# Kernel optimization log

Measured on AMD Instinct MI355X. Metric: run time of the kernel, lower is better.

Reference implementation:

```python
import jax, jax.numpy as jnp
import numpy as np

DIM = 1024
N_HEADS = 16


def setup_inputs() -> dict:
    key = jax.random.key(0)
    ks = jax.random.split(key, 7)
    x = jax.random.normal(ks[0], (2, 2048, DIM), dtype=jnp.float32)
    wq = jax.random.normal(ks[1], (DIM, DIM), dtype=jnp.float32) * 0.01
    wk = jax.random.normal(ks[2], (DIM, DIM), dtype=jnp.float32) * 0.01
    wv = jax.random.normal(ks[3], (DIM, DIM), dtype=jnp.float32) * 0.01
    wo = jax.random.normal(ks[4], (DIM, DIM), dtype=jnp.float32) * 0.01
    w1 = jax.random.normal(ks[5], (DIM, 4 * DIM), dtype=jnp.float32) * 0.01
    w2 = jax.random.normal(ks[6], (4 * DIM, DIM), dtype=jnp.float32) * 0.01
    return {"x": x, "wq": wq, "wk": wk, "wv": wv, "wo": wo, "w1": w1, "w2": w2}


def reference(x, wq, wk, wv, wo, w1, w2):
    bsz, seqlen, dim = x.shape
    head_dim = dim // N_HEADS
    # project and split heads: [b, h, s, d]
    q = (x @ wq).reshape(bsz, seqlen, N_HEADS, head_dim).transpose(0, 2, 1, 3)
    k = (x @ wk).reshape(bsz, seqlen, N_HEADS, head_dim).transpose(0, 2, 1, 3)
    v = (x @ wv).reshape(bsz, seqlen, N_HEADS, head_dim).transpose(0, 2, 1, 3)
    scale = head_dim ** (-0.5)
    # full [b, h, s, s] score matrix, as in the original module
    attn = jnp.einsum('bhqd,bhkd->bhqk', q, k) * scale
    attn = jax.nn.softmax(attn, axis=-1)
    out = jnp.einsum('bhqk,bhkd->bhqd', attn, v)
    out = out.transpose(0, 2, 1, 3).reshape(bsz, seqlen, dim)
    x = x + out @ wo
    h = jax.nn.relu(x @ w1)
    x = x + h @ w2
    return x
```

## Files before the change

kernel.cpp:

```cpp
#include <hip/hip_runtime.h>
#include <hip/hip_bf16.h>
#include <stdint.h>

typedef __attribute__((ext_vector_type(8))) short short8_t;
typedef __attribute__((ext_vector_type(4))) short short4_t;
typedef __attribute__((ext_vector_type(4))) float floatx4;

#define MTOT 4096
#define DIMV 1024
#define SEQ  2048
#define NH   16
#define HD   64
#define QKV_LD 3072
#define KVB 64
#define NKT (SEQ / KVB)

__device__ __forceinline__ floatx4 mfma16(short8_t a, short8_t b, floatx4 c) {
    return __builtin_amdgcn_mfma_f32_16x16x32_bf16(a, b, c, 0, 0, 0);
}

__device__ __forceinline__ void gload_lds16(const void* g, void* l) {
    __builtin_amdgcn_global_load_lds(
        (const __attribute__((address_space(1))) void*)g,
        (__attribute__((address_space(3))) void*)l,
        16, 0, 0);
}

__device__ __forceinline__ short bf16bits(float f) {
    return __builtin_bit_cast(short, __float2bfloat16(f));
}

__device__ __forceinline__ short8_t frag64(const __hip_bfloat16* base, int row, int col0) {
    int off = row * 64 + (((col0 >> 3) ^ (row & 7)) << 3);
    return *(const short8_t*)(base + off);
}

struct bf4 { __hip_bfloat16 a, b, c, d; };

__global__ void prep_all(const float* __restrict__ x,
                         const float* __restrict__ wq, const float* __restrict__ wk,
                         const float* __restrict__ wv, const float* __restrict__ wo,
                         const float* __restrict__ w1, const float* __restrict__ w2,
                         __hip_bfloat16* __restrict__ xb,
                         __hip_bfloat16* __restrict__ wqkvt, __hip_bfloat16* __restrict__ wot,
                         __hip_bfloat16* __restrict__ w1t, __hip_bfloat16* __restrict__ w2t) {
    __shared__ float tile[32][33];
    int bid = blockIdx.x;
    int t = threadIdx.x;
    if (bid >= 12288) {
        int i = (bid - 12288) * 256 + t;
        const float4* xv = reinterpret_cast<const float4*>(x) + i;
        float4 v = *xv;
        bf4 r;
        r.a = __float2bfloat16(v.x); r.b = __float2bfloat16(v.y);
        r.c = __float2bfloat16(v.z); r.d = __float2bfloat16(v.w);
        *reinterpret_cast<bf4*>(xb + (size_t)i * 4) = r;
        return;
    }
    const float* w; __hip_bfloat16* wt; int K, N, K32, tau; float scale = 1.0f;
    if (bid < 1024)      { w = wq; wt = wqkvt;                 K = 1024; N = 1024; K32 = 32;  tau = bid;        scale = 0.125f; }
    else if (bid < 2048) { w = wk; wt = wqkvt + 1024 * 1024;   K = 1024; N = 1024; K32 = 32;  tau = bid - 1024; }
    else if (bid < 3072) { w = wv; wt = wqkvt + 2048 * 1024;   K = 1024; N = 1024; K32 = 32;  tau = bid - 2048; }
    else if (bid < 4096) { w = wo; wt = wot;                   K = 1024; N = 1024; K32 = 32;  tau = bid - 3072; }
    else if (bid < 8192) { w = w1; wt = w1t;                   K = 1024; N = 4096; K32 = 32;  tau = bid - 4096; }
    else                 { w = w2; wt = w2t;                   K = 4096; N = 1024; K32 = 128; tau = bid - 8192; }
    int k0 = (tau % K32) * 32, n0 = (tau / K32) * 32;
    int tx = t & 31, ty = t >> 5;
    #pragma unroll
    for (int r = 0; r < 32; r += 8)
        tile[ty + r][tx] = w[(size_t)(k0 + ty + r) * N + n0 + tx];
    __syncthreads();
    #pragma unroll
    for (int r = 0; r < 32; r += 8)
        wt[(size_t)(n0 + ty + r) * K + k0 + tx] = __float2bfloat16(tile[tx][ty + r] * scale);
}

__global__ void vtrans(const __hip_bfloat16* __restrict__ v, int ld,
                       __hip_bfloat16* __restrict__ vt) {
    __shared__ __hip_bfloat16 tile[32][33];
    int s0 = blockIdx.x * 32;
    int c0 = blockIdx.y * 32;
    int tx = threadIdx.x & 31, ty = threadIdx.x >> 5;
    #pragma unroll
    for (int r = 0; r < 32; r += 8)
        tile[ty + r][tx] = v[(size_t)(s0 + ty + r) * ld + c0 + tx];
    __syncthreads();
    int b = s0 >> 11;
    int h = c0 >> 6;
    int d0 = c0 & 63;
    #pragma unroll
    for (int r = 0; r < 32; r += 8)
        vt[(size_t)((b * NH + h) * HD + d0 + ty + r) * SEQ + (s0 & 2047) + tx] = tile[tx][ty + r];
}

__global__ void combine2(const float* __restrict__ p0, const float* __restrict__ p1,
                         const float* __restrict__ resid, float* __restrict__ out, int n4) {
    int i = blockIdx.x * 256 + threadIdx.x;
    if (i < n4) {
        float4 a = reinterpret_cast<const float4*>(p0)[i];
        float4 b = reinterpret_cast<const float4*>(p1)[i];
        float4 c = reinterpret_cast<const float4*>(resid)[i];
        float4 r;
        r.x = a.x + b.x + c.x; r.y = a.y + b.y + c.y;
        r.z = a.z + b.z + c.z; r.w = a.w + b.w + c.w;
        reinterpret_cast<float4*>(out)[i] = r;
    }
}

template <int EPI>
__launch_bounds__(256)
__global__ void gemm_bt(const __hip_bfloat16* __restrict__ A,
                        const __hip_bfloat16* __restrict__ Bt,
                        int M, int N, int K, int lda, int ldb, float scale,
                        const float* __restrict__ resid,
                        float* __restrict__ outf,
                        __hip_bfloat16* __restrict__ outb, size_t zout) {
    __shared__ __align__(16) __hip_bfloat16 As[3][128 * 32];
    __shared__ __align__(16) __hip_bfloat16 Bs[3][128 * 32];
    A += (size_t)blockIdx.z * K;
    Bt += (size_t)blockIdx.z * K;
    outf += (size_t)blockIdx.z * zout;
    const int t = threadIdx.x;
    const int l = t & 63;
    const int w = t >> 6;
    const int wr = w >> 1, wc = w & 1;
    const int lrow = l & 15;
    const int lk = (l >> 4) << 3;
    const int li4 = (l >> 4) << 2;
    const int arow0 = blockIdx.x * 128;
    const int brow0 = blockIdx.y * 128;

    floatx4 acc[4][4];
    #pragma unroll
    for (int m = 0; m < 4; m++)
        #pragma unroll
        for (int n = 0; n < 4; n++)
            acc[m][n] = (floatx4){0.f, 0.f, 0.f, 0.f};

    const int nkt = K >> 5;
    const int sr = t >> 2, sc8 = (t & 3) << 3;
    const __hip_bfloat16* ga0 = A + (size_t)(arow0 + sr) * lda + sc8;
    const __hip_bfloat16* gb0 = Bt + (size_t)(brow0 + sr) * ldb + sc8;

#define GSTAGE(KT, BUF) do { \
        const __hip_bfloat16* ga_ = ga0 + (KT) * 32; \
        const __hip_bfloat16* gb_ = gb0 + (KT) * 32; \
        gload_lds16(ga_,                    (char*)As[BUF] + t * 16); \
        gload_lds16(ga_ + (size_t)64 * lda, (char*)As[BUF] + 4096 + t * 16); \
        gload_lds16(gb_,                    (char*)Bs[BUF] + t * 16); \
        gload_lds16(gb_ + (size_t)64 * ldb, (char*)Bs[BUF] + 4096 + t * 16); \
    } while (0)

    GSTAGE(0, 0);
    GSTAGE(1, 1);
    asm volatile("s_waitcnt vmcnt(4)" ::: "memory");
    __builtin_amdgcn_s_barrier();
    __builtin_amdgcn_sched_barrier(0);

    for (int kt = 0; kt < nkt; ++kt) {
        const int cur = kt % 3;
        if (kt + 2 < nkt) GSTAGE(kt + 2, (kt + 2) % 3);
        short8_t af[4], bfr[4];
        #pragma unroll
        for (int m = 0; m < 4; m++)
            af[m] = *(const short8_t*)((const char*)As[cur] + (((wr << 6) + (m << 4) + lrow) << 6) + (lk << 1));
        #pragma unroll
        for (int n = 0; n < 4; n++)
            bfr[n] = *(const short8_t*)((const char*)Bs[cur] + (((wc << 6) + (n << 4) + lrow) << 6) + (lk << 1));
        #pragma unroll
        for (int m = 0; m < 4; m++)
            #pragma unroll
            for (int n = 0; n < 4; n++)
                acc[m][n] = mfma16(af[m], bfr[n], acc[m][n]);
        if (kt + 2 < nkt) asm volatile("s_waitcnt vmcnt(4)" ::: "memory");
        else              asm volatile("s_waitcnt vmcnt(0)" ::: "memory");
        __builtin_amdgcn_s_barrier();
        __builtin_amdgcn_sched_barrier(0);
    }
#undef GSTAGE

    #pragma unroll
    for (int m = 0; m < 4; m++) {
        #pragma unroll
        for (int n = 0; n < 4; n++) {
            int row = arow0 + (wr << 6) + (m << 4) + li4;
            int col = brow0 + (wc << 6) + (n << 4) + lrow;
            #pragma unroll
            for (int i = 0; i < 4; i++) {
                float vv = acc[m][n][i] * scale;
                size_t off = (size_t)(row + i) * N + col;
                if (EPI == 0) {
                    outb[off] = __float2bfloat16(vv);
                } else if (EPI == 1) {
                    outb[off] = __float2bfloat16(vv > 0.f ? vv : 0.f);
                } else if (EPI == 2) {
                    float f = vv + resid[off];
                    outf[off] = f;
                    outb[off] = __float2bfloat16(f);
                } else if (EPI == 3) {
                    outf[off] = vv + resid[off];
                } else {
                    outf[off] = vv;
                }
            }
        }
    }
}

__launch_bounds__(256, 4)
__global__ void attn_kernel(const __hip_bfloat16* __restrict__ qkv,
                            const __hip_bfloat16* __restrict__ vt,
                            __hip_bfloat16* __restrict__ o) {
    __shared__ __align__(16) __hip_bfloat16 Ks[2][KVB * 64];
    __shared__ __align__(16) __hip_bfloat16 Vs[2][KVB * 64];
    __shared__ __align__(16) __hip_bfloat16 Ps[64 * 64];
    const int t = threadIdx.x, l = t & 63, w = t >> 6;
    const int bh = blockIdx.y;
    const int b = bh >> 4, h = bh & 15;
    const int q0 = blockIdx.x * 64;
    const int lq = l & 15;
    const int lg = l >> 4;

    const __hip_bfloat16* qbase = qkv + (size_t)(b * SEQ + q0) * QKV_LD + h * HD;
    const __hip_bfloat16* kbase = qkv + (size_t)(b * SEQ) * QKV_LD + 1024 + h * HD;
    const __hip_bfloat16* vbase = vt + (size_t)(bh * HD) * SEQ;

    #pragma unroll
    for (int s = 0; s < 2; ++s) {
        int u = t + 256 * s;
        int r = u >> 3, c = (u & 7) ^ (r & 7);
        gload_lds16(qbase + (size_t)r * QKV_LD + c * 8, (char*)Ps + u * 16);
        gload_lds16(kbase + (size_t)r * QKV_LD + c * 8, (char*)Ks[0] + u * 16);
        gload_lds16(vbase + (size_t)r * SEQ + c * 8,    (char*)Vs[0] + u * 16);
    }
    asm volatile("s_waitcnt vmcnt(0)" ::: "memory");
    __builtin_amdgcn_s_barrier();
    __builtin_amdgcn_sched_barrier(0);

    short8_t qf[2];
    #pragma unroll
    for (int kc = 0; kc < 2; kc++)
        qf[kc] = frag64(Ps, (w << 4) + lq, kc * 32 + lg * 8);
    asm volatile("s_waitcnt lgkmcnt(0)" ::: "memory");
    __builtin_amdgcn_s_barrier();
    __builtin_amdgcn_sched_barrier(0);

    float l_part = 0.f;
    floatx4 o_acc[4];
    #pragma unroll
    for (int n = 0; n < 4; n++)
        o_acc[n] = (floatx4){0.f, 0.f, 0.f, 0.f};

    int cur = 0;
    for (int kt = 0; kt < NKT; ++kt) {
        if (kt + 1 < NKT) {
            int kv = (kt + 1) * KVB;
            #pragma unroll
            for (int s = 0; s < 2; ++s) {
                int u = t + 256 * s;
                int r = u >> 3, c = (u & 7) ^ (r & 7);
                gload_lds16(kbase + (size_t)(kv + r) * QKV_LD + c * 8,
                            (char*)Ks[cur ^ 1] + u * 16);
                gload_lds16(vbase + (size_t)r * SEQ + kv + c * 8,
                            (char*)Vs[cur ^ 1] + u * 16);
            }
        }

        const __hip_bfloat16* kcb = Ks[cur];
        floatx4 sa[4];
        #pragma unroll
        for (int n = 0; n < 4; n++)
            sa[n] = (floatx4){0.f, 0.f, 0.f, 0.f};
        #pragma unroll
        for (int n = 0; n < 4; n++) {
            #pragma unroll
            for (int kc = 0; kc < 2; kc++) {
                short8_t kf = frag64(kcb, n * 16 + lq, kc * 32 + lg * 8);
                sa[n] = mfma16(kf, qf[kc], sa[n]);
            }
        }

        short4_t pk[4];
        #pragma unroll
        for (int n = 0; n < 4; n++) {
            float p0 = __expf(sa[n][0]);
            float p1 = __expf(sa[n][1]);
            float p2 = __expf(sa[n][2]);
            float p3 = __expf(sa[n][3]);
            l_part += (p0 + p1) + (p2 + p3);
            short4_t pv;
            pv[0] = bf16bits(p0);
            pv[1] = bf16bits(p1);
            pv[2] = bf16bits(p2);
            pv[3] = bf16bits(p3);
            pk[n] = pv;
        }

        {
            int row = (w << 4) + lq;
            int rowb = row * 128;
            int rw = row & 7;
            #pragma unroll
            for (int n = 0; n < 4; n++) {
                int k0 = n * 16 + lg * 4;
                char* dst = (char*)Ps + rowb +
                            ((((k0 >> 3) ^ rw) << 4) | ((k0 & 4) << 1));
                *(short4_t*)dst = pk[n];
            }
        }
        asm volatile("s_waitcnt lgkmcnt(0)" ::: "memory");
        __builtin_amdgcn_sched_barrier(0);

        const __hip_bfloat16* vcb = Vs[cur];
        #pragma unroll
        for (int kc = 0; kc < 2; kc++) {
            short8_t pf = frag64(Ps, (w << 4) + lq, kc * 32 + lg * 8);
            #pragma unroll
            for (int n = 0; n < 4; n++) {
                short8_t vf = frag64(vcb, n * 16 + lq, kc * 32 + lg * 8);
                o_acc[n] = mfma16(pf, vf, o_acc[n]);
            }
        }
        asm volatile("s_waitcnt vmcnt(0)" ::: "memory");
        __builtin_amdgcn_s_barrier();
        __builtin_amdgcn_sched_barrier(0);
        cur ^= 1;
    }

    __hip_bfloat16* obase = o + (size_t)(b * SEQ + q0) * DIMV + h * HD;
    float lr = l_part;
    lr += __shfl_xor(lr, 16, 64);
    lr += __shfl_xor(lr, 32, 64);
    #pragma unroll
    for (int i = 0; i < 4; i++) {
        float li = 1.0f / __shfl(lr, (lg << 2) + i, 16);
        int row = (w << 4) + (lg << 2) + i;
        #pragma unroll
        for (int n = 0; n < 4; n++) {
            obase[(size_t)row * DIMV + n * 16 + lq] =
                __float2bfloat16(o_acc[n][i] * li);
        }
    }
}

extern "C" void kernel_launch(void* const* d_in, const int* in_sizes, int n_in,
                              void* d_out, int out_size, void* d_ws, size_t ws_size,
                              hipStream_t stream) {
    const float* x  = (const float*)d_in[0];
    const float* wq = (const float*)d_in[1];
    const float* wk = (const float*)d_in[2];
    const float* wv = (const float*)d_in[3];
    const float* wo = (const float*)d_in[4];
    const float* w1 = (const float*)d_in[5];
    const float* w2 = (const float*)d_in[6];
    float* outf = (float*)d_out;

    char* ws = (char*)d_ws;
    const size_t MB = (size_t)1 << 20;
    __hip_bfloat16* xb    = (__hip_bfloat16*)(ws + 0 * MB);
    __hip_bfloat16* wqkvt = (__hip_bfloat16*)(ws + 8 * MB);
    __hip_bfloat16* wot   = (__hip_bfloat16*)(ws + 14 * MB);
    __hip_bfloat16* w1t   = (__hip_bfloat16*)(ws + 16 * MB);
    __hip_bfloat16* w2t   = (__hip_bfloat16*)(ws + 24 * MB);
    __hip_bfloat16* qkvb  = (__hip_bfloat16*)(ws + 32 * MB);
    __hip_bfloat16* vtp   = (__hip_bfloat16*)(ws + 56 * MB);
    __hip_bfloat16* atb   = (__hip_bfloat16*)(ws + 64 * MB);
    __hip_bfloat16* x1b   = (__hip_bfloat16*)(ws + 72 * MB);
    __hip_bfloat16* hb    = (__hip_bfloat16*)(ws + 80 * MB);
    float* part0 = (float*)(ws + 32 * MB);

    prep_all<<<dim3(16384), dim3(256), 0, stream>>>(x, wq, wk, wv, wo, w1, w2,
                                                    xb, wqkvt, wot, w1t, w2t);

    gemm_bt<0><<<dim3(32, 24), dim3(256), 0, stream>>>(xb, wqkvt, MTOT, QKV_LD, 1024,
                                                       1024, 1024, 1.0f, nullptr, nullptr, qkvb, 0);
    vtrans<<<dim3(128, 32), dim3(256), 0, stream>>>(qkvb + 2048, QKV_LD, vtp);

    attn_kernel<<<dim3(32, 32), dim3(256), 0, stream>>>(qkvb, vtp, atb);

    gemm_bt<2><<<dim3(32, 8), dim3(256), 0, stream>>>(atb, wot, MTOT, 1024, 1024,
                                                      1024, 1024, 1.0f, x, outf, x1b, 0);
    gemm_bt<1><<<dim3(32, 32), dim3(256), 0, stream>>>(x1b, w1t, MTOT, 4096, 1024,
                                                       1024, 1024, 1.0f, nullptr, nullptr, hb, 0);
    gemm_bt<4><<<dim3(32, 8, 2), dim3(256), 0, stream>>>(hb, w2t, MTOT, 1024, 2048,
                                                         4096, 4096, 1.0f, nullptr, part0, nullptr,
                                                         (size_t)MTOT * 1024);
    combine2<<<dim3(4096), dim3(256), 0, stream>>>(part0, part0 + (size_t)MTOT * 1024,
                                                   outf, outf, MTOT * 1024 / 4);
}
```

Measured before the change: 340.9 us.

## Add 256x256-tile GEMM for QKV and FFN1, fold log2e into Q scale

```diff
diff --git a/kernel.cpp b/kernel.cpp
--- a/kernel.cpp
+++ b/kernel.cpp
@@ -14,6 +14,7 @@
 #define QKV_LD 3072
 #define KVB 64
 #define NKT (SEQ / KVB)
+#define LOG2E 1.44269504088896340736f
 
 __device__ __forceinline__ floatx4 mfma16(short8_t a, short8_t b, floatx4 c) {
     return __builtin_amdgcn_mfma_f32_16x16x32_bf16(a, b, c, 0, 0, 0);
@@ -58,7 +59,7 @@
         return;
     }
     const float* w; __hip_bfloat16* wt; int K, N, K32, tau; float scale = 1.0f;
-    if (bid < 1024)      { w = wq; wt = wqkvt;                 K = 1024; N = 1024; K32 = 32;  tau = bid;        scale = 0.125f; }
+    if (bid < 1024)      { w = wq; wt = wqkvt;                 K = 1024; N = 1024; K32 = 32;  tau = bid;        scale = 0.125f * LOG2E; }
     else if (bid < 2048) { w = wk; wt = wqkvt + 1024 * 1024;   K = 1024; N = 1024; K32 = 32;  tau = bid - 1024; }
     else if (bid < 3072) { w = wv; wt = wqkvt + 2048 * 1024;   K = 1024; N = 1024; K32 = 32;  tau = bid - 2048; }
     else if (bid < 4096) { w = wo; wt = wot;                   K = 1024; N = 1024; K32 = 32;  tau = bid - 3072; }
@@ -104,6 +105,107 @@
         r.x = a.x + b.x + c.x; r.y = a.y + b.y + c.y;
         r.z = a.z + b.z + c.z; r.w = a.w + b.w + c.w;
         reinterpret_cast<float4*>(out)[i] = r;
+    }
+}
+
+template <int EPI>
+__launch_bounds__(512)
+__global__ void gemm256(const __hip_bfloat16* __restrict__ A,
+                        const __hip_bfloat16* __restrict__ Bt,
+                        int N, int K, int lda, int ldb,
+                        __hip_bfloat16* __restrict__ outb) {
+    __shared__ __align__(16) __hip_bfloat16 As[2][256 * 64];
+    __shared__ __align__(16) __hip_bfloat16 Bs[2][256 * 64];
+    const int t = threadIdx.x;
+    const int l = t & 63;
+    const int w = t >> 6;
+    const int wr = w >> 2;
+    const int wc = w & 3;
+    const int lq = l & 15;
+    const int lk = (l >> 4) << 3;
+    const int li4 = (l >> 4) << 2;
+    const int arow0 = blockIdx.x * 256;
+    const int brow0 = blockIdx.y * 256;
+
+    floatx4 acc[8][4];
+    #pragma unroll
+    for (int m = 0; m < 8; m++)
+        #pragma unroll
+        for (int n = 0; n < 4; n++)
+            acc[m][n] = (floatx4){0.f, 0.f, 0.f, 0.f};
+
+    const int sr_ = t >> 3;
+    const int sc_ = ((t & 7) ^ ((t >> 3) & 7));
+    const __hip_bfloat16* ga0 = A + (size_t)(arow0 + sr_) * lda + sc_ * 8;
+    const __hip_bfloat16* gb0 = Bt + (size_t)(brow0 + sr_) * ldb + sc_ * 8;
+
+#define STG_A(BUF, S, KT) gload_lds16(ga0 + (size_t)(64 * (S)) * lda + (KT) * 64, \
+                                      (char*)As[BUF] + (t + 512 * (S)) * 16)
+#define STG_B(BUF, S, KT) gload_lds16(gb0 + (size_t)(64 * (S)) * ldb + (KT) * 64, \
+                                      (char*)Bs[BUF] + (t + 512 * (S)) * 16)
+
+    const int nkt = K >> 6;
+    #pragma unroll
+    for (int s = 0; s < 4; ++s) { STG_A(0, s, 0); STG_B(0, s, 0); }
+    asm volatile("s_waitcnt vmcnt(0)" ::: "memory");
+    __builtin_amdgcn_s_barrier();
+    __builtin_amdgcn_sched_barrier(0);
+
+    for (int kt = 0; kt < nkt; ++kt) {
+        const int cur = kt & 1;
+        const bool pre = (kt + 1 < nkt);
+        #pragma unroll
+        for (int p = 0; p < 4; ++p) {
+            const int mh = p >> 1, nh = p & 1;
+            short8_t af[4][2], bf[2][2];
+            #pragma unroll
+            for (int mi = 0; mi < 4; mi++)
+                #pragma unroll
+                for (int kc = 0; kc < 2; kc++)
+                    af[mi][kc] = frag64(As[cur], wr * 128 + (mh * 4 + mi) * 16 + lq, kc * 32 + lk);
+            #pragma unroll
+            for (int ni = 0; ni < 2; ni++)
+                #pragma unroll
+                for (int kc = 0; kc < 2; kc++)
+                    bf[ni][kc] = frag64(Bs[cur], wc * 64 + (nh * 2 + ni) * 16 + lq, kc * 32 + lk);
+            if (pre) { STG_A(cur ^ 1, p, kt + 1); STG_B(cur ^ 1, p, kt + 1); }
+            __builtin_amdgcn_s_barrier();
+            asm volatile("s_waitcnt lgkmcnt(0)" ::: "memory");
+            __builtin_amdgcn_sched_barrier(0);
+            __builtin_amdgcn_s_setprio(1);
+            #pragma unroll
+            for (int kc = 0; kc < 2; kc++)
+                #pragma unroll
+                for (int mi = 0; mi < 4; mi++)
+                    #pragma unroll
+                    for (int ni = 0; ni < 2; ni++)
+                        acc[mh * 4 + mi][nh * 2 + ni] =
+                            mfma16(af[mi][kc], bf[ni][kc], acc[mh * 4 + mi][nh * 2 + ni]);
+            __builtin_amdgcn_s_setprio(0);
+            if (p == 3) {
+                if (pre) asm volatile("s_waitcnt vmcnt(0)" ::: "memory");
+            }
+            __builtin_amdgcn_s_barrier();
+            __builtin_amdgcn_sched_barrier(0);
+        }
+    }
+#undef STG_A
+#undef STG_B
+
+    #pragma unroll
+    for (int m = 0; m < 8; m++) {
+        #pragma unroll
+        for (int n = 0; n < 4; n++) {
+            int row = arow0 + wr * 128 + m * 16 + li4;
+            int col = brow0 + wc * 64 + n * 16 + lq;
+            #pragma unroll
+            for (int i = 0; i < 4; i++) {
+                float vv = acc[m][n][i];
+                size_t off = (size_t)(row + i) * N + col;
+                if (EPI == 0) outb[off] = __float2bfloat16(vv);
+                else          outb[off] = __float2bfloat16(vv > 0.f ? vv : 0.f);
+            }
+        }
     }
 }
 
@@ -191,14 +293,10 @@
                 size_t off = (size_t)(row + i) * N + col;
                 if (EPI == 0) {
                     outb[off] = __float2bfloat16(vv);
-                } else if (EPI == 1) {
-                    outb[off] = __float2bfloat16(vv > 0.f ? vv : 0.f);
                 } else if (EPI == 2) {
                     float f = vv + resid[off];
                     outf[off] = f;
                     outb[off] = __float2bfloat16(f);
-                } else if (EPI == 3) {
-                    outf[off] = vv + resid[off];
                 } else {
                     outf[off] = vv;
                 }
@@ -283,10 +381,10 @@
         short4_t pk[4];
         #pragma unroll
         for (int n = 0; n < 4; n++) {
-            float p0 = __expf(sa[n][0]);
-            float p1 = __expf(sa[n][1]);
-            float p2 = __expf(sa[n][2]);
-            float p3 = __expf(sa[n][3]);
+            float p0 = exp2f(sa[n][0]);
+            float p1 = exp2f(sa[n][1]);
+            float p2 = exp2f(sa[n][2]);
+            float p3 = exp2f(sa[n][3]);
             l_part += (p0 + p1) + (p2 + p3);
             short4_t pv;
             pv[0] = bf16bits(p0);
@@ -372,16 +470,14 @@
     prep_all<<<dim3(16384), dim3(256), 0, stream>>>(x, wq, wk, wv, wo, w1, w2,
                                                     xb, wqkvt, wot, w1t, w2t);
 
-    gemm_bt<0><<<dim3(32, 24), dim3(256), 0, stream>>>(xb, wqkvt, MTOT, QKV_LD, 1024,
-                                                       1024, 1024, 1.0f, nullptr, nullptr, qkvb, 0);
+    gemm256<0><<<dim3(16, 12), dim3(512), 0, stream>>>(xb, wqkvt, QKV_LD, 1024, 1024, 1024, qkvb);
     vtrans<<<dim3(128, 32), dim3(256), 0, stream>>>(qkvb + 2048, QKV_LD, vtp);
 
     attn_kernel<<<dim3(32, 32), dim3(256), 0, stream>>>(qkvb, vtp, atb);
 
     gemm_bt<2><<<dim3(32, 8), dim3(256), 0, stream>>>(atb, wot, MTOT, 1024, 1024,
                                                       1024, 1024, 1.0f, x, outf, x1b, 0);
-    gemm_bt<1><<<dim3(32, 32), dim3(256), 0, stream>>>(x1b, w1t, MTOT, 4096, 1024,
-                                                       1024, 1024, 1.0f, nullptr, nullptr, hb, 0);
+    gemm256<1><<<dim3(16, 16), dim3(512), 0, stream>>>(x1b, w1t, 4096, 1024, 1024, 1024, hb);
     gemm_bt<4><<<dim3(32, 8, 2), dim3(256), 0, stream>>>(hb, w2t, MTOT, 1024, 2048,
                                                          4096, 4096, 1.0f, nullptr, part0, nullptr,
                                                          (size_t)MTOT * 1024);
```

Result: no change. 346.3 us (+1.6%).
